# Kernel optimization log

Measured on AMD Instinct MI355X. Metric: run time of the kernel, lower is better.

The kernel has to match this reference:

```python
import jax, jax.numpy as jnp
import numpy as np

BN_EPS = 1e-5      # nn.BatchNorm1d default in MLP_Block
DICE_EPS = 1e-8    # Dice's BatchNorm eps


def _bn(x, gamma, beta, eps):
    # training-mode BatchNorm1d over the batch axis (biased variance, like torch)
    m = jnp.mean(x, axis=0)
    v = jnp.var(x, axis=0)
    return gamma * (x - m) * jax.lax.rsqrt(v + eps) + beta


def _dice(x, gamma, beta, alpha):
    gate = jax.nn.sigmoid(_bn(x, gamma, beta, DICE_EPS))
    return gate * x + (1.0 - gate) * alpha * x


def setup_inputs() -> dict:
    key = jax.random.key(0)
    ks = jax.random.split(key, 12)
    B, S, E = 4096, 200, 64
    D_in, H1, H2 = 4 * E, 64, 32
    inp = {
        "query": jax.random.normal(ks[0], (B, 1, E), jnp.float32),
        "facts": jax.random.normal(ks[1], (B, S, E), jnp.float32),
        "mask": jax.random.randint(ks[2], (B, S, 1), 0, 2).astype(jnp.int32),
        # layer 1: Linear(256->64) + BN + Dice
        "W1": jax.random.normal(ks[3], (D_in, H1), jnp.float32) / np.sqrt(D_in),
        "b1": jnp.zeros((H1,), jnp.float32),
        "g1": jnp.ones((H1,), jnp.float32),
        "be1": jnp.zeros((H1,), jnp.float32),
        "dg1": jnp.ones((H1,), jnp.float32),
        "db1": jnp.zeros((H1,), jnp.float32),
        "a1": 0.1 * jax.random.normal(ks[4], (H1,), jnp.float32),
        # layer 2: Linear(64->32) + BN + Dice
        "W2": jax.random.normal(ks[5], (H1, H2), jnp.float32) / np.sqrt(H1),
        "b2": jnp.zeros((H2,), jnp.float32),
        "g2": jnp.ones((H2,), jnp.float32),
        "be2": jnp.zeros((H2,), jnp.float32),
        "dg2": jnp.ones((H2,), jnp.float32),
        "db2": jnp.zeros((H2,), jnp.float32),
        "a2": 0.1 * jax.random.normal(ks[6], (H2,), jnp.float32),
        # final fc: Linear(32->1)
        "Wf": jax.random.normal(ks[7], (H2, 1), jnp.float32) / np.sqrt(H2),
        "bf": jnp.zeros((1,), jnp.float32),
    }
    return inp


def reference(query, facts, mask,
              W1, b1, g1, be1, dg1, db1, a1,
              W2, b2, g2, be2, dg2, db2, a2,
              Wf, bf):
    B, S, E = facts.shape
    q = jnp.broadcast_to(query, (B, S, E))
    # [B*S, 4E]
    ai = jnp.concatenate([q, facts, q - facts, q * facts], axis=-1).reshape(-1, 4 * E)
    h = ai @ W1 + b1
    h = _bn(h, g1, be1, BN_EPS)
    h = _dice(h, dg1, db1, a1)
    h = h @ W2 + b2
    h = _bn(h, g2, be2, BN_EPS)
    h = _dice(h, dg2, db2, a2)
    scores = (h @ Wf + bf).reshape(B, S, 1)
    scores = jnp.where(mask > 0, scores, jnp.float32(-1e9))
    weights = jax.nn.softmax(scores, axis=1)          # [B,S,1]
    return jnp.sum(weights * facts, axis=1)           # [B,E]
```

## Files before the change

### kernel.cpp

```cpp
#include <hip/hip_runtime.h>
#include <hip/hip_bf16.h>

#define NB 4096
#define NS 200
#define NE 64
#define NROWS (NB*NS)

typedef __attribute__((ext_vector_type(8))) short bf16x8;
typedef __attribute__((ext_vector_type(4))) float f32x4;

__device__ __forceinline__ float bf2f(unsigned v) {
    return __uint_as_float(v << 16);
}
__device__ __forceinline__ unsigned f2bf(float x) {
    unsigned u = __float_as_uint(x);
    u = u + 0x7fffu + ((u >> 16) & 1u);
    return u >> 16;
}

__global__ __launch_bounds__(256) void k_prep(const float* __restrict__ W2,
                                              float* __restrict__ stats,
                                              unsigned short* __restrict__ W2h,
                                              unsigned short* __restrict__ W2l) {
    const int t = threadIdx.x, bb = blockIdx.x;
    if (bb < 144) { stats[bb*256 + t] = 0.f; return; }
    #pragma unroll
    for (int r = 0; r < 8; ++r) {
        int idx = r*256 + t;
        int k = idx >> 5, j = idx & 31;
        float v = W2[idx];
        unsigned hb = f2bf(v);
        W2h[j*64 + k] = (unsigned short)hb;
        W2l[j*64 + k] = (unsigned short)(__float_as_uint(v - bf2f(hb)) >> 16);
    }
}

__global__ __launch_bounds__(256) void k_mq(const float* __restrict__ query,
        const float* __restrict__ W1, const float* __restrict__ b1,
        unsigned* __restrict__ Mt, float* __restrict__ qW) {
    __shared__ float qs[8][64];
    const int t = threadIdx.x;
    const int b0 = blockIdx.x * 8;
    qs[t >> 6][t & 63]       = query[(size_t)b0*64 + t];
    qs[4 + (t >> 6)][t & 63] = query[(size_t)b0*64 + 256 + t];
    __syncthreads();
    const int j = t >> 2, e0 = (t & 3) * 16;
    const int P = ((j>>5)&1)*32 + ((j>>2)&1)*16 + ((j>>3)&3)*4 + (j&3);
    float dW[16], sW[16], w3[16];
    #pragma unroll
    for (int ee = 0; ee < 16; ++ee) {
        const int e = e0 + ee;
        float w0  = W1[(size_t)e*64 + j];
        float w1v = W1[(size_t)(64+e)*64 + j];
        float w2v = W1[(size_t)(128+e)*64 + j];
        w3[ee]    = W1[(size_t)(192+e)*64 + j];
        dW[ee] = w1v - w2v;
        sW[ee] = w0 + w2v;
    }
    const float bj = b1[j];
    #pragma unroll
    for (int bb = 0; bb < 8; ++bb) {
        const int b = b0 + bb;
        float qp = 0.f;
        unsigned wbuf[8];
        #pragma unroll
        for (int ee = 0; ee < 16; ee += 2) {
            float q0 = qs[bb][e0+ee], q1 = qs[bb][e0+ee+1];
            float m0 = fmaf(q0, w3[ee],   dW[ee]);
            float m1 = fmaf(q1, w3[ee+1], dW[ee+1]);
            qp = fmaf(q0, sW[ee],   qp);
            qp = fmaf(q1, sW[ee+1], qp);
            wbuf[ee >> 1] = f2bf(m0) | (f2bf(m1) << 16);
        }
        uint4* dst = (uint4*)(Mt + (size_t)b*2048 + P*32 + (t & 3)*8);
        dst[0] = make_uint4(wbuf[0], wbuf[1], wbuf[2], wbuf[3]);
        dst[1] = make_uint4(wbuf[4], wbuf[5], wbuf[6], wbuf[7]);
        qp += __shfl_xor(qp, 1, 64);
        qp += __shfl_xor(qp, 2, 64);
        if ((t & 3) == 0) qW[(size_t)b*64 + P] = bj + qp;
    }
}

__device__ __forceinline__ void cvt_hilo(const float4& x, const float4& y,
                                         bf16x8& hi, bf16x8& lo) {
    const float f[8] = {x.x, x.y, x.z, x.w, y.x, y.y, y.z, y.w};
    #pragma unroll
    for (int i = 0; i < 8; ++i) {
        unsigned us = f2bf(f[i]);
        hi[i] = (short)us;
        lo[i] = (short)(__float_as_uint(f[i] - bf2f(us)) >> 16);
    }
}

__device__ __forceinline__ void p1_tile(
    const float4& x0, const float4& x1, const float4& x2, const float4& x3,
    const bf16x8 (&Af)[4][2], const float4 (&qw4)[4],
    int sv, bool chk, float (&sacc)[16], float (&qacc)[16],
    unsigned* __restrict__ hb, int h)
{
    bf16x8 Bh0, Bl0, Bh1, Bl1;
    cvt_hilo(x0, x1, Bh0, Bl0);
    cvt_hilo(x2, x3, Bh1, Bl1);
    f32x4 acc[4];
    #pragma unroll
    for (int cg = 0; cg < 4; ++cg) {
        acc[cg] = (f32x4){0.f,0.f,0.f,0.f};
        acc[cg] = __builtin_amdgcn_mfma_f32_16x16x32_bf16(Af[cg][0], Bh0, acc[cg], 0,0,0);
        acc[cg] = __builtin_amdgcn_mfma_f32_16x16x32_bf16(Af[cg][1], Bh1, acc[cg], 0,0,0);
        acc[cg] = __builtin_amdgcn_mfma_f32_16x16x32_bf16(Af[cg][0], Bl0, acc[cg], 0,0,0);
        acc[cg] = __builtin_amdgcn_mfma_f32_16x16x32_bf16(Af[cg][1], Bl1, acc[cg], 0,0,0);
    }
    if (!chk || sv < 200) {
        float v[4][4];
        #pragma unroll
        for (int cg = 0; cg < 4; ++cg) {
            v[cg][0] = acc[cg][0] + qw4[cg].x;
            v[cg][1] = acc[cg][1] + qw4[cg].y;
            v[cg][2] = acc[cg][2] + qw4[cg].z;
            v[cg][3] = acc[cg][3] + qw4[cg].w;
            #pragma unroll
            for (int r = 0; r < 4; ++r) {
                sacc[cg*4+r] += v[cg][r];
                qacc[cg*4+r] = fmaf(v[cg][r], v[cg][r], qacc[cg*4+r]);
            }
        }
        uint4 c0, c1;
        c0.x = f2bf(v[0][0]) | (f2bf(v[0][1]) << 16);
        c0.y = f2bf(v[0][2]) | (f2bf(v[0][3]) << 16);
        c0.z = f2bf(v[1][0]) | (f2bf(v[1][1]) << 16);
        c0.w = f2bf(v[1][2]) | (f2bf(v[1][3]) << 16);
        c1.x = f2bf(v[2][0]) | (f2bf(v[2][1]) << 16);
        c1.y = f2bf(v[2][2]) | (f2bf(v[2][3]) << 16);
        c1.z = f2bf(v[3][0]) | (f2bf(v[3][1]) << 16);
        c1.w = f2bf(v[3][2]) | (f2bf(v[3][3]) << 16);
        *(uint4*)&hb[(size_t)sv*32 + 4*h]      = c0;
        *(uint4*)&hb[(size_t)sv*32 + 16 + 4*h] = c1;
    }
}

__global__ __launch_bounds__(256) void k_p1g(const float* __restrict__ facts,
        const unsigned* __restrict__ Mt, const float* __restrict__ qW,
        float* __restrict__ gsumS, float* __restrict__ gsqS,
        unsigned* __restrict__ h1w) {
    __shared__ float sred[4][128];
    const int b = blockIdx.x, t = threadIdx.x;
    const int l = t & 63, w = t >> 6;
    const int lo4 = l & 15, h = l >> 4;

    const unsigned* mb = Mt + (size_t)b*2048;
    bf16x8 Af[4][2];
    #pragma unroll
    for (int cg = 0; cg < 4; ++cg)
        #pragma unroll
        for (int ks = 0; ks < 2; ++ks)
            Af[cg][ks] = *(const bf16x8*)&mb[(cg*16 + lo4)*32 + ks*16 + 4*h];
    float4 qw4[4];
    #pragma unroll
    for (int cg = 0; cg < 4; ++cg)
        qw4[cg] = *(const float4*)&qW[(size_t)b*64 + cg*16 + 4*h];

    const float* fb = facts + (size_t)b*(NS*NE) + 8*h;
    unsigned* hb = h1w + (size_t)b*200*32;

    float sacc[16], qacc[16];
    #pragma unroll
    for (int i = 0; i < 16; ++i) { sacc[i] = 0.f; qacc[i] = 0.f; }

#define P1L(RT, X0, X1, X2, X3, CHK) do { \
    const int sv_ = (RT)*16 + lo4; \
    if (!(CHK) || sv_ < 200) { \
        const float* p_ = fb + (size_t)sv_*64; \
        X0 = *(const float4*)(p_);      X1 = *(const float4*)(p_+4); \
        X2 = *(const float4*)(p_+32);   X3 = *(const float4*)(p_+36); \
    } else { X0 = X1 = X2 = X3 = make_float4(0.f,0.f,0.f,0.f); } \
} while(0)
#define P1P(RT, X0, X1, X2, X3, CHK) \
    p1_tile(X0, X1, X2, X3, Af, qw4, (RT)*16 + lo4, CHK, sacc, qacc, hb, h)

    float4 A0,A1,A2,A3, B0,B1,B2,B3, C0,C1,C2_,C3;
    const bool h3 = (w == 0);
    P1L(w,     A0,A1,A2,A3, false);
    P1L(w + 4, B0,B1,B2,B3, false);
    P1L(w + 8, C0,C1,C2_,C3, false);
    P1P(w,     A0,A1,A2,A3, false);
    if (h3) P1L(12, A0,A1,A2,A3, true);
    P1P(w + 4, B0,B1,B2,B3, false);
    P1P(w + 8, C0,C1,C2_,C3, false);
    if (h3) P1P(12, A0,A1,A2,A3, true);
#undef P1L
#undef P1P

    #pragma unroll
    for (int cg = 0; cg < 4; ++cg) {
        #pragma unroll
        for (int r = 0; r < 4; ++r) {
            const int i = cg*4 + r;
            float s = sacc[i], q = qacc[i];
            s += __shfl_xor(s, 1, 64); s += __shfl_xor(s, 2, 64);
            s += __shfl_xor(s, 4, 64); s += __shfl_xor(s, 8, 64);
            q += __shfl_xor(q, 1, 64); q += __shfl_xor(q, 2, 64);
            q += __shfl_xor(q, 4, 64); q += __shfl_xor(q, 8, 64);
            if (lo4 == 0) {
                const int ch = 32*(cg>>1) + 4*(cg&1) + 8*h + r;
                sred[w][ch] = s; sred[w][64 + ch] = q;
            }
        }
    }
    __syncthreads();
    if (t < 128) {
        const int slot = b & 255;
        float v = sred[0][t] + sred[1][t] + sred[2][t] + sred[3][t];
        if (t < 64) atomicAdd(gsumS + slot*64 + t, v);
        else        atomicAdd(gsqS  + slot*64 + (t - 64), v);
    }
}

__global__ __launch_bounds__(64) void k_fin(const float* __restrict__ gsumS,
        const float* __restrict__ gsqS, int S,
        const float* __restrict__ gam, const float* __restrict__ bet,
        const float* __restrict__ dg, const float* __restrict__ db,
        float* __restrict__ C, int n) {
    int j = threadIdx.x;
    if (j >= n) return;
    float sum = 0.f, sq = 0.f;
    #pragma unroll 8
    for (int s = 0; s < S; ++s) {
        sum += gsumS[s*n + j];
        sq  += gsqS[s*n + j];
    }
    const float Ninv = 1.0f / (float)NROWS;
    float m = sum * Ninv;
    float v = fmaxf(sq*Ninv - m*m, 0.f);
    float rstd = rsqrtf(v + 1e-5f);
    float A = gam[j] * rstd;
    float Bc = bet[j] - A*m;
    float vard = A*A*v;
    float rstdd = rsqrtf(vard + 1e-8f);
    float G = dg[j] * rstdd * A;
    float H = db[j] - G*m;
    C[j] = A; C[n+j] = Bc; C[2*n+j] = G; C[3*n+j] = H;
}

__device__ __forceinline__ void dice8(const bf16x8& hv, int k0, const float* Cs,
                                      bf16x8& Bh, bf16x8& Bl) {
    #pragma unroll
    for (int i = 0; i < 8; ++i) {
        const int k = k0 + i;
        float h = bf2f((unsigned short)hv[i]);
        float x  = fmaf(Cs[k],     h, Cs[64+k]);
        float tg = fmaf(Cs[128+k], h, Cs[192+k]);
        float gate = __builtin_amdgcn_rcpf(1.f + __expf(-tg));
        float fac = fmaf(gate, Cs[256+k], Cs[320+k]);
        float hd = x * fac;
        unsigned us = f2bf(hd);
        Bh[i] = (short)us;
        Bl[i] = (short)(__float_as_uint(hd - bf2f(us)) >> 16);
    }
}

__global__ __launch_bounds__(256) void k_pass2(const unsigned short* __restrict__ h1u,
        const float* __restrict__ C1, const float* __restrict__ a1,
        const unsigned short* __restrict__ W2h, const unsigned short* __restrict__ W2l,
        const float* __restrict__ b2,
        unsigned* __restrict__ h2w,
        float* __restrict__ gsum2S, float* __restrict__ gsq2S) {
    __shared__ float Cs[384];
    __shared__ float sred[4][64];
    const int t = threadIdx.x;
    const int l = t & 63, w = t >> 6;
    const int lo4 = l & 15, hi4 = l >> 4;
    Cs[t] = C1[t];
    if (t < 64) { Cs[256 + t] = 1.f - a1[t]; Cs[320 + t] = a1[t]; }
    __syncthreads();

    bf16x8 Ah[2][2], Al[2][2];
    #pragma unroll
    for (int cg = 0; cg < 2; ++cg) {
        const int col = cg*16 + lo4;
        #pragma unroll
        for (int ks = 0; ks < 2; ++ks) {
            const int k0 = ks*32 + 8*hi4;
            Ah[cg][ks] = *(const bf16x8*)&W2h[col*64 + k0];
            Al[cg][ks] = *(const bf16x8*)&W2l[col*64 + k0];
        }
    }
    float4 b24[2];
    #pragma unroll
    for (int cg = 0; cg < 2; ++cg)
        b24[cg] = *(const float4*)&b2[cg*16 + 4*hi4];

    float s2[8], q2[8];
    #pragma unroll
    for (int i = 0; i < 8; ++i) { s2[i] = 0.f; q2[i] = 0.f; }
    const int rbase0 = blockIdx.x*256 + w*64;

#define P2_LOAD(TT, H0, H1) do { \
    const int s_ = rbase0 + (TT)*16 + lo4; \
    H0 = *(const bf16x8*)&h1u[(size_t)s_*64 + 8*hi4]; \
    H1 = *(const bf16x8*)&h1u[(size_t)s_*64 + 32 + 8*hi4]; \
} while(0)

#define P2_PROC(TT, H0, H1) do { \
    bf16x8 Bh0, Bl0, Bh1, Bl1; \
    dice8(H0, 8*hi4,      Cs, Bh0, Bl0); \
    dice8(H1, 32 + 8*hi4, Cs, Bh1, Bl1); \
    f32x4 a_[2]; \
    _Pragma("unroll") \
    for (int cg = 0; cg < 2; ++cg) { \
        a_[cg] = (f32x4){0.f,0.f,0.f,0.f}; \
        a_[cg] = __builtin_amdgcn_mfma_f32_16x16x32_bf16(Ah[cg][0], Bh0, a_[cg], 0,0,0); \
        a_[cg] = __builtin_amdgcn_mfma_f32_16x16x32_bf16(Ah[cg][1], Bh1, a_[cg], 0,0,0); \
        a_[cg] = __builtin_amdgcn_mfma_f32_16x16x32_bf16(Al[cg][0], Bh0, a_[cg], 0,0,0); \
        a_[cg] = __builtin_amdgcn_mfma_f32_16x16x32_bf16(Al[cg][1], Bh1, a_[cg], 0,0,0); \
        a_[cg] = __builtin_amdgcn_mfma_f32_16x16x32_bf16(Ah[cg][0], Bl0, a_[cg], 0,0,0); \
        a_[cg] = __builtin_amdgcn_mfma_f32_16x16x32_bf16(Ah[cg][1], Bl1, a_[cg], 0,0,0); \
    } \
    const int s_ = rbase0 + (TT)*16 + lo4; \
    _Pragma("unroll") \
    for (int cg = 0; cg < 2; ++cg) { \
        float v0 = a_[cg][0] + b24[cg].x; \
        float v1 = a_[cg][1] + b24[cg].y; \
        float v2 = a_[cg][2] + b24[cg].z; \
        float v3 = a_[cg][3] + b24[cg].w; \
        s2[cg*4+0] += v0; q2[cg*4+0] = fmaf(v0, v0, q2[cg*4+0]); \
        s2[cg*4+1] += v1; q2[cg*4+1] = fmaf(v1, v1, q2[cg*4+1]); \
        s2[cg*4+2] += v2; q2[cg*4+2] = fmaf(v2, v2, q2[cg*4+2]); \
        s2[cg*4+3] += v3; q2[cg*4+3] = fmaf(v3, v3, q2[cg*4+3]); \
        uint2 pv; \
        pv.x = f2bf(v0) | (f2bf(v1) << 16); \
        pv.y = f2bf(v2) | (f2bf(v3) << 16); \
        *(uint2*)&h2w[(size_t)s_*16 + 8*cg + 2*hi4] = pv; \
    } \
} while(0)

    bf16x8 X0, X1, Y0, Y1;
    P2_LOAD(0, X0, X1);
    P2_LOAD(1, Y0, Y1);
    P2_PROC(0, X0, X1);
    P2_LOAD(2, X0, X1);
    P2_PROC(1, Y0, Y1);
    P2_LOAD(3, Y0, Y1);
    P2_PROC(2, X0, X1);
    P2_PROC(3, Y0, Y1);
#undef P2_LOAD
#undef P2_PROC

    #pragma unroll
    for (int i = 0; i < 8; ++i) {
        float s = s2[i], q = q2[i];
        s += __shfl_xor(s, 1, 64); s += __shfl_xor(s, 2, 64);
        s += __shfl_xor(s, 4, 64); s += __shfl_xor(s, 8, 64);
        q += __shfl_xor(q, 1, 64); q += __shfl_xor(q, 2, 64);
        q += __shfl_xor(q, 4, 64); q += __shfl_xor(q, 8, 64);
        if (lo4 == 0) {
            const int ch = (i >> 2)*16 + 4*hi4 + (i & 3);
            sred[w][ch] = s; sred[w][32 + ch] = q;
        }
    }
    __syncthreads();
    if (t < 64) {
        const int slot = blockIdx.x & 63;
        float v = sred[0][t] + sred[1][t] + sred[2][t] + sred[3][t];
        if (t < 32) atomicAdd(gsum2S + slot*32 + t, v);
        else        atomicAdd(gsq2S  + slot*32 + (t - 32), v);
    }
}

__device__ __forceinline__ float wsum(float v) {
    #pragma unroll
    for (int m = 32; m; m >>= 1) v += __shfl_xor(v, m, 64);
    return v;
}
__device__ __forceinline__ float wmax(float v) {
    #pragma unroll
    for (int m = 32; m; m >>= 1) v = fmaxf(v, __shfl_xor(v, m, 64));
    return v;
}
__global__ __launch_bounds__(256) void k_pass3(const unsigned* __restrict__ h2p,
        const float* __restrict__ C2, const float* __restrict__ a2,
        const float* __restrict__ Wf, const float* __restrict__ bfp,
        const int* __restrict__ mask, const float* __restrict__ facts,
        float* __restrict__ out) {
    __shared__ float rmax[4], rsum[4], wgt[256], par[4][64];
    const int b = blockIdx.x, t = threadIdx.x;
    float score = -1e30f;
    if (t < NS) {
        size_t g = (size_t)b*NS + t;
        const uint4* hv = (const uint4*)(h2p + g*16);
        uint4 U0 = hv[0], U1 = hv[1], U2 = hv[2], U3 = hv[3];
        unsigned uw[16] = {U0.x,U0.y,U0.z,U0.w, U1.x,U1.y,U1.z,U1.w,
                           U2.x,U2.y,U2.z,U2.w, U3.x,U3.y,U3.z,U3.w};
        float acc = bfp[0];
        #pragma unroll
        for (int jp = 0; jp < 16; ++jp) {
            unsigned u = uw[jp];
            #pragma unroll
            for (int h = 0; h < 2; ++h) {
                int k = 2*jp + h;
                float hval = bf2f(h ? (u >> 16) : (u & 0xffffu));
                float x  = fmaf(C2[k],    hval, C2[32+k]);
                float tg = fmaf(C2[64+k], hval, C2[96+k]);
                float gate = __builtin_amdgcn_rcpf(1.f + __expf(-tg));
                float al = a2[k];
                acc = fmaf(x * fmaf(gate, 1.f - al, al), Wf[k], acc);
            }
        }
        score = (mask[g] > 0) ? acc : -1e9f;
    }
    float m = wmax(score);
    if ((t & 63) == 0) rmax[t >> 6] = m;
    __syncthreads();
    m = fmaxf(fmaxf(rmax[0],rmax[1]), fmaxf(rmax[2],rmax[3]));
    float ee = __expf(score - m);
    float zs = wsum(ee);
    if ((t & 63) == 0) rsum[t >> 6] = zs;
    __syncthreads();
    float Z = rsum[0]+rsum[1]+rsum[2]+rsum[3];
    wgt[t] = ee * __builtin_amdgcn_rcpf(Z);
    __syncthreads();
    const int e = t & 63, p = t >> 6;
    const float* fbp = facts + (size_t)b*(NS*NE) + e;
    float a0 = 0.f, a1 = 0.f;
    #pragma unroll
    for (int i = 0; i < 200; i += 8) {
        a0 = fmaf(wgt[p + i],     fbp[(size_t)(p + i)*64],     a0);
        a1 = fmaf(wgt[p + i + 4], fbp[(size_t)(p + i + 4)*64], a1);
    }
    par[p][e] = a0 + a1;
    __syncthreads();
    if (t < 64) out[(size_t)b*64 + t] = par[0][t]+par[1][t]+par[2][t]+par[3][t];
}

extern "C" void kernel_launch(void* const* d_in, const int* in_sizes, int n_in,
                              void* d_out, int out_size, void* d_ws, size_t ws_size,
                              hipStream_t stream) {
    const float* query = (const float*)d_in[0];
    const float* facts = (const float*)d_in[1];
    const int*   mask  = (const int*)d_in[2];
    const float* W1  = (const float*)d_in[3];
    const float* b1  = (const float*)d_in[4];
    const float* g1  = (const float*)d_in[5];
    const float* be1 = (const float*)d_in[6];
    const float* dg1 = (const float*)d_in[7];
    const float* db1 = (const float*)d_in[8];
    const float* a1  = (const float*)d_in[9];
    const float* W2  = (const float*)d_in[10];
    const float* b2  = (const float*)d_in[11];
    const float* g2  = (const float*)d_in[12];
    const float* be2 = (const float*)d_in[13];
    const float* dg2 = (const float*)d_in[14];
    const float* db2 = (const float*)d_in[15];
    const float* a2  = (const float*)d_in[16];
    const float* Wf  = (const float*)d_in[17];
    const float* bff = (const float*)d_in[18];
    float* out = (float*)d_out;

    float* ws = (float*)d_ws;
    float* gsum1s = ws + 0;
    float* gsq1s  = ws + 16384;
    float* gsum2s = ws + 32768;
    float* gsq2s  = ws + 34816;
    float* C1     = ws + 36864;
    float* C2     = ws + 37120;
    unsigned short* W2h = (unsigned short*)(ws + 37376);
    unsigned short* W2l = (unsigned short*)(ws + 38400);
    unsigned* h1p = (unsigned*)(ws + 40960);
    unsigned* h2p = h1p + (size_t)NROWS*32;
    unsigned* Mt = h2p;
    float* qWb   = (float*)(h2p + (size_t)NB*2048);
    (void)ws_size; (void)in_sizes; (void)n_in; (void)out_size;

    k_prep<<<145, 256, 0, stream>>>(W2, ws, W2h, W2l);
    k_mq<<<NB/8, 256, 0, stream>>>(query, W1, b1, Mt, qWb);
    k_p1g<<<NB, 256, 0, stream>>>(facts, Mt, qWb, gsum1s, gsq1s, h1p);
    k_fin<<<1, 64, 0, stream>>>(gsum1s, gsq1s, 256, g1, be1, dg1, db1, C1, 64);
    k_pass2<<<NROWS/256, 256, 0, stream>>>((const unsigned short*)h1p, C1, a1,
                                           W2h, W2l, b2,
                                           h2p, gsum2s, gsq2s);
    k_fin<<<1, 32, 0, stream>>>(gsum2s, gsq2s, 64, g2, be2, dg2, db2, C2, 32);
    k_pass3<<<NB, 256, 0, stream>>>(h2p, C2, a2, Wf, bff, mask, facts, out);
}
```

Baseline: 217.0 us.

## Recompute layer-1 activations in pass 2 instead of storing h1

The first pass now only accumulates BatchNorm statistics for layer 1 and no longer writes the bf16 h1 intermediate. The second pass re-reads facts per batch, recomputes the layer-1 matmul with MFMA, applies BN+Dice, and then does layer 2. This trades the write and re-read of h1 (about 105 MB each way) for an extra read of facts (about 210 MB) plus duplicated MFMA and conversion work. The workspace layout shrinks accordingly.

```diff
diff --git a/kernel.cpp b/kernel.cpp
--- a/kernel.cpp
+++ b/kernel.cpp
@@ -92,11 +92,10 @@
     }
 }
 
-__device__ __forceinline__ void p1_tile(
+__device__ __forceinline__ void p1s_tile(
     const float4& x0, const float4& x1, const float4& x2, const float4& x3,
-    const bf16x8 (&Af)[4][2], const float4 (&qw4)[4],
-    int sv, bool chk, float (&sacc)[16], float (&qacc)[16],
-    unsigned* __restrict__ hb, int h)
+    const bf16x8 (&Af)[4][2], const f32x4 (&qw4)[4],
+    int sv, bool chk, float (&sacc)[16], float (&qacc)[16])
 {
     bf16x8 Bh0, Bl0, Bh1, Bl1;
     cvt_hilo(x0, x1, Bh0, Bl0);
@@ -111,37 +110,21 @@
         acc[cg] = __builtin_amdgcn_mfma_f32_16x16x32_bf16(Af[cg][1], Bl1, acc[cg], 0,0,0);
     }
     if (!chk || sv < 200) {
-        float v[4][4];
         #pragma unroll
         for (int cg = 0; cg < 4; ++cg) {
-            v[cg][0] = acc[cg][0] + qw4[cg].x;
-            v[cg][1] = acc[cg][1] + qw4[cg].y;
-            v[cg][2] = acc[cg][2] + qw4[cg].z;
-            v[cg][3] = acc[cg][3] + qw4[cg].w;
             #pragma unroll
             for (int r = 0; r < 4; ++r) {
-                sacc[cg*4+r] += v[cg][r];
-                qacc[cg*4+r] = fmaf(v[cg][r], v[cg][r], qacc[cg*4+r]);
+                float v = acc[cg][r] + qw4[cg][r];
+                sacc[cg*4+r] += v;
+                qacc[cg*4+r] = fmaf(v, v, qacc[cg*4+r]);
             }
         }
-        uint4 c0, c1;
-        c0.x = f2bf(v[0][0]) | (f2bf(v[0][1]) << 16);
-        c0.y = f2bf(v[0][2]) | (f2bf(v[0][3]) << 16);
-        c0.z = f2bf(v[1][0]) | (f2bf(v[1][1]) << 16);
-        c0.w = f2bf(v[1][2]) | (f2bf(v[1][3]) << 16);
-        c1.x = f2bf(v[2][0]) | (f2bf(v[2][1]) << 16);
-        c1.y = f2bf(v[2][2]) | (f2bf(v[2][3]) << 16);
-        c1.z = f2bf(v[3][0]) | (f2bf(v[3][1]) << 16);
-        c1.w = f2bf(v[3][2]) | (f2bf(v[3][3]) << 16);
-        *(uint4*)&hb[(size_t)sv*32 + 4*h]      = c0;
-        *(uint4*)&hb[(size_t)sv*32 + 16 + 4*h] = c1;
-    }
-}
-
-__global__ __launch_bounds__(256) void k_p1g(const float* __restrict__ facts,
+    }
+}
+
+__global__ __launch_bounds__(256) void k_p1s(const float* __restrict__ facts,
         const unsigned* __restrict__ Mt, const float* __restrict__ qW,
-        float* __restrict__ gsumS, float* __restrict__ gsqS,
-        unsigned* __restrict__ h1w) {
+        float* __restrict__ gsumS, float* __restrict__ gsqS) {
     __shared__ float sred[4][128];
     const int b = blockIdx.x, t = threadIdx.x;
     const int l = t & 63, w = t >> 6;
@@ -154,13 +137,12 @@
         #pragma unroll
         for (int ks = 0; ks < 2; ++ks)
             Af[cg][ks] = *(const bf16x8*)&mb[(cg*16 + lo4)*32 + ks*16 + 4*h];
-    float4 qw4[4];
+    f32x4 qw4[4];
     #pragma unroll
     for (int cg = 0; cg < 4; ++cg)
-        qw4[cg] = *(const float4*)&qW[(size_t)b*64 + cg*16 + 4*h];
+        qw4[cg] = *(const f32x4*)&qW[(size_t)b*64 + cg*16 + 4*h];
 
     const float* fb = facts + (size_t)b*(NS*NE) + 8*h;
-    unsigned* hb = h1w + (size_t)b*200*32;
 
     float sacc[16], qacc[16];
     #pragma unroll
@@ -175,7 +157,7 @@
     } else { X0 = X1 = X2 = X3 = make_float4(0.f,0.f,0.f,0.f); } \
 } while(0)
 #define P1P(RT, X0, X1, X2, X3, CHK) \
-    p1_tile(X0, X1, X2, X3, Af, qw4, (RT)*16 + lo4, CHK, sacc, qacc, hb, h)
+    p1s_tile(X0, X1, X2, X3, Af, qw4, (RT)*16 + lo4, CHK, sacc, qacc)
 
     float4 A0,A1,A2,A3, B0,B1,B2,B3, C0,C1,C2_,C3;
     const bool h3 = (w == 0);
@@ -241,24 +223,8 @@
     C[j] = A; C[n+j] = Bc; C[2*n+j] = G; C[3*n+j] = H;
 }
 
-__device__ __forceinline__ void dice8(const bf16x8& hv, int k0, const float* Cs,
-                                      bf16x8& Bh, bf16x8& Bl) {
-    #pragma unroll
-    for (int i = 0; i < 8; ++i) {
-        const int k = k0 + i;
-        float h = bf2f((unsigned short)hv[i]);
-        float x  = fmaf(Cs[k],     h, Cs[64+k]);
-        float tg = fmaf(Cs[128+k], h, Cs[192+k]);
-        float gate = __builtin_amdgcn_rcpf(1.f + __expf(-tg));
-        float fac = fmaf(gate, Cs[256+k], Cs[320+k]);
-        float hd = x * fac;
-        unsigned us = f2bf(hd);
-        Bh[i] = (short)us;
-        Bl[i] = (short)(__float_as_uint(hd - bf2f(us)) >> 16);
-    }
-}
-
-__global__ __launch_bounds__(256) void k_pass2(const unsigned short* __restrict__ h1u,
+__global__ __launch_bounds__(256) void k_p2f(const float* __restrict__ facts,
+        const unsigned* __restrict__ Mt, const float* __restrict__ qW,
         const float* __restrict__ C1, const float* __restrict__ a1,
         const unsigned short* __restrict__ W2h, const unsigned short* __restrict__ W2l,
         const float* __restrict__ b2,
@@ -266,84 +232,137 @@
         float* __restrict__ gsum2S, float* __restrict__ gsq2S) {
     __shared__ float Cs[384];
     __shared__ float sred[4][64];
-    const int t = threadIdx.x;
+    const int b = blockIdx.x, t = threadIdx.x;
     const int l = t & 63, w = t >> 6;
-    const int lo4 = l & 15, hi4 = l >> 4;
+    const int lo4 = l & 15, h = l >> 4;
     Cs[t] = C1[t];
     if (t < 64) { Cs[256 + t] = 1.f - a1[t]; Cs[320 + t] = a1[t]; }
     __syncthreads();
 
-    bf16x8 Ah[2][2], Al[2][2];
+    const unsigned* mb = Mt + (size_t)b*2048;
+    bf16x8 Af[4][2];
+    #pragma unroll
+    for (int cg = 0; cg < 4; ++cg)
+        #pragma unroll
+        for (int ks = 0; ks < 2; ++ks)
+            Af[cg][ks] = *(const bf16x8*)&mb[(cg*16 + lo4)*32 + ks*16 + 4*h];
+    f32x4 qw4[4];
+    #pragma unroll
+    for (int cg = 0; cg < 4; ++cg)
+        qw4[cg] = *(const f32x4*)&qW[(size_t)b*64 + cg*16 + 4*h];
+
+    bf16x8 Wh[2][2], Wl[2][2];
     #pragma unroll
     for (int cg = 0; cg < 2; ++cg) {
         const int col = cg*16 + lo4;
         #pragma unroll
         for (int ks = 0; ks < 2; ++ks) {
-            const int k0 = ks*32 + 8*hi4;
-            Ah[cg][ks] = *(const bf16x8*)&W2h[col*64 + k0];
-            Al[cg][ks] = *(const bf16x8*)&W2l[col*64 + k0];
-        }
-    }
-    float4 b24[2];
+            const int k0 = ks*32 + 8*h;
+            Wh[cg][ks] = *(const bf16x8*)&W2h[col*64 + k0];
+            Wl[cg][ks] = *(const bf16x8*)&W2l[col*64 + k0];
+        }
+    }
+    f32x4 b24[2];
     #pragma unroll
     for (int cg = 0; cg < 2; ++cg)
-        b24[cg] = *(const float4*)&b2[cg*16 + 4*hi4];
+        b24[cg] = *(const f32x4*)&b2[cg*16 + 4*h];
+
+    const float* fb = facts + (size_t)b*(NS*NE) + 8*h;
+    unsigned* h2b = h2w + (size_t)b*200*16;
 
     float s2[8], q2[8];
     #pragma unroll
     for (int i = 0; i < 8; ++i) { s2[i] = 0.f; q2[i] = 0.f; }
-    const int rbase0 = blockIdx.x*256 + w*64;
-
-#define P2_LOAD(TT, H0, H1) do { \
-    const int s_ = rbase0 + (TT)*16 + lo4; \
-    H0 = *(const bf16x8*)&h1u[(size_t)s_*64 + 8*hi4]; \
-    H1 = *(const bf16x8*)&h1u[(size_t)s_*64 + 32 + 8*hi4]; \
+
+#define P2L(RT, X0, X1, X2, X3, CHK) do { \
+    const int sv_ = (RT)*16 + lo4; \
+    if (!(CHK) || sv_ < 200) { \
+        const float* p_ = fb + (size_t)sv_*64; \
+        X0 = *(const float4*)(p_);      X1 = *(const float4*)(p_+4); \
+        X2 = *(const float4*)(p_+32);   X3 = *(const float4*)(p_+36); \
+    } else { X0 = X1 = X2 = X3 = make_float4(0.f,0.f,0.f,0.f); } \
 } while(0)
 
-#define P2_PROC(TT, H0, H1) do { \
-    bf16x8 Bh0, Bl0, Bh1, Bl1; \
-    dice8(H0, 8*hi4,      Cs, Bh0, Bl0); \
-    dice8(H1, 32 + 8*hi4, Cs, Bh1, Bl1); \
+#define P2P(RT, X0, X1, X2, X3, CHK) do { \
+    bf16x8 Fh0, Fl0, Fh1, Fl1; \
+    cvt_hilo(X0, X1, Fh0, Fl0); \
+    cvt_hilo(X2, X3, Fh1, Fl1); \
+    f32x4 acc[4]; \
+    _Pragma("unroll") \
+    for (int cg = 0; cg < 4; ++cg) { \
+        acc[cg] = (f32x4){0.f,0.f,0.f,0.f}; \
+        acc[cg] = __builtin_amdgcn_mfma_f32_16x16x32_bf16(Af[cg][0], Fh0, acc[cg], 0,0,0); \
+        acc[cg] = __builtin_amdgcn_mfma_f32_16x16x32_bf16(Af[cg][1], Fh1, acc[cg], 0,0,0); \
+        acc[cg] = __builtin_amdgcn_mfma_f32_16x16x32_bf16(Af[cg][0], Fl0, acc[cg], 0,0,0); \
+        acc[cg] = __builtin_amdgcn_mfma_f32_16x16x32_bf16(Af[cg][1], Fl1, acc[cg], 0,0,0); \
+    } \
+    bf16x8 H0h, H0l, H1h, H1l; \
+    _Pragma("unroll") \
+    for (int cg = 0; cg < 4; ++cg) { \
+        const int cb = 32*(cg>>1) + 4*(cg&1) + 8*h; \
+        f32x4 Ac = *(const f32x4*)&Cs[cb]; \
+        f32x4 Bc = *(const f32x4*)&Cs[64+cb]; \
+        f32x4 Gc = *(const f32x4*)&Cs[128+cb]; \
+        f32x4 Hc = *(const f32x4*)&Cs[192+cb]; \
+        f32x4 Oc = *(const f32x4*)&Cs[256+cb]; \
+        f32x4 Lc = *(const f32x4*)&Cs[320+cb]; \
+        _Pragma("unroll") \
+        for (int r = 0; r < 4; ++r) { \
+            float hv = acc[cg][r] + qw4[cg][r]; \
+            float x  = fmaf(Ac[r], hv, Bc[r]); \
+            float tg = fmaf(Gc[r], hv, Hc[r]); \
+            float gate = __builtin_amdgcn_rcpf(1.f + __expf(-tg)); \
+            float hd = x * fmaf(gate, Oc[r], Lc[r]); \
+            unsigned us = f2bf(hd); \
+            unsigned lo = __float_as_uint(hd - bf2f(us)) >> 16; \
+            const int idx = 4*(cg&1) + r; \
+            if (cg < 2) { H0h[idx] = (short)us; H0l[idx] = (short)lo; } \
+            else        { H1h[idx] = (short)us; H1l[idx] = (short)lo; } \
+        } \
+    } \
     f32x4 a_[2]; \
     _Pragma("unroll") \
     for (int cg = 0; cg < 2; ++cg) { \
         a_[cg] = (f32x4){0.f,0.f,0.f,0.f}; \
-        a_[cg] = __builtin_amdgcn_mfma_f32_16x16x32_bf16(Ah[cg][0], Bh0, a_[cg], 0,0,0); \
-        a_[cg] = __builtin_amdgcn_mfma_f32_16x16x32_bf16(Ah[cg][1], Bh1, a_[cg], 0,0,0); \
-        a_[cg] = __builtin_amdgcn_mfma_f32_16x16x32_bf16(Al[cg][0], Bh0, a_[cg], 0,0,0); \
-        a_[cg] = __builtin_amdgcn_mfma_f32_16x16x32_bf16(Al[cg][1], Bh1, a_[cg], 0,0,0); \
-        a_[cg] = __builtin_amdgcn_mfma_f32_16x16x32_bf16(Ah[cg][0], Bl0, a_[cg], 0,0,0); \
-        a_[cg] = __builtin_amdgcn_mfma_f32_16x16x32_bf16(Ah[cg][1], Bl1, a_[cg], 0,0,0); \
+        a_[cg] = __builtin_amdgcn_mfma_f32_16x16x32_bf16(Wh[cg][0], H0h, a_[cg], 0,0,0); \
+        a_[cg] = __builtin_amdgcn_mfma_f32_16x16x32_bf16(Wh[cg][1], H1h, a_[cg], 0,0,0); \
+        a_[cg] = __builtin_amdgcn_mfma_f32_16x16x32_bf16(Wl[cg][0], H0h, a_[cg], 0,0,0); \
+        a_[cg] = __builtin_amdgcn_mfma_f32_16x16x32_bf16(Wl[cg][1], H1h, a_[cg], 0,0,0); \
+        a_[cg] = __builtin_amdgcn_mfma_f32_16x16x32_bf16(Wh[cg][0], H0l, a_[cg], 0,0,0); \
+        a_[cg] = __builtin_amdgcn_mfma_f32_16x16x32_bf16(Wh[cg][1], H1l, a_[cg], 0,0,0); \
     } \
-    const int s_ = rbase0 + (TT)*16 + lo4; \
-    _Pragma("unroll") \
-    for (int cg = 0; cg < 2; ++cg) { \
-        float v0 = a_[cg][0] + b24[cg].x; \
-        float v1 = a_[cg][1] + b24[cg].y; \
-        float v2 = a_[cg][2] + b24[cg].z; \
-        float v3 = a_[cg][3] + b24[cg].w; \
-        s2[cg*4+0] += v0; q2[cg*4+0] = fmaf(v0, v0, q2[cg*4+0]); \
-        s2[cg*4+1] += v1; q2[cg*4+1] = fmaf(v1, v1, q2[cg*4+1]); \
-        s2[cg*4+2] += v2; q2[cg*4+2] = fmaf(v2, v2, q2[cg*4+2]); \
-        s2[cg*4+3] += v3; q2[cg*4+3] = fmaf(v3, v3, q2[cg*4+3]); \
-        uint2 pv; \
-        pv.x = f2bf(v0) | (f2bf(v1) << 16); \
-        pv.y = f2bf(v2) | (f2bf(v3) << 16); \
-        *(uint2*)&h2w[(size_t)s_*16 + 8*cg + 2*hi4] = pv; \
+    const int sv_ = (RT)*16 + lo4; \
+    if (!(CHK) || sv_ < 200) { \
+        _Pragma("unroll") \
+        for (int cg = 0; cg < 2; ++cg) { \
+            float v0 = a_[cg][0] + b24[cg][0]; \
+            float v1 = a_[cg][1] + b24[cg][1]; \
+            float v2 = a_[cg][2] + b24[cg][2]; \
+            float v3 = a_[cg][3] + b24[cg][3]; \
+            s2[cg*4+0] += v0; q2[cg*4+0] = fmaf(v0, v0, q2[cg*4+0]); \
+            s2[cg*4+1] += v1; q2[cg*4+1] = fmaf(v1, v1, q2[cg*4+1]); \
+            s2[cg*4+2] += v2; q2[cg*4+2] = fmaf(v2, v2, q2[cg*4+2]); \
+            s2[cg*4+3] += v3; q2[cg*4+3] = fmaf(v3, v3, q2[cg*4+3]); \
+            uint2 pv; \
+            pv.x = f2bf(v0) | (f2bf(v1) << 16); \
+            pv.y = f2bf(v2) | (f2bf(v3) << 16); \
+            *(uint2*)&h2b[(size_t)sv_*16 + 8*cg + 2*h] = pv; \
+        } \
     } \
 } while(0)
 
-    bf16x8 X0, X1, Y0, Y1;
-    P2_LOAD(0, X0, X1);
-    P2_LOAD(1, Y0, Y1);
-    P2_PROC(0, X0, X1);
-    P2_LOAD(2, X0, X1);
-    P2_PROC(1, Y0, Y1);
-    P2_LOAD(3, Y0, Y1);
-    P2_PROC(2, X0, X1);
-    P2_PROC(3, Y0, Y1);
-#undef P2_LOAD
-#undef P2_PROC
+    float4 A0,A1,A2,A3, B0,B1,B2,B3;
+    const bool h3 = (w == 0);
+    P2L(w,     A0,A1,A2,A3, false);
+    P2L(w + 4, B0,B1,B2,B3, false);
+    P2P(w,     A0,A1,A2,A3, false);
+    P2L(w + 8, A0,A1,A2,A3, false);
+    P2P(w + 4, B0,B1,B2,B3, false);
+    if (h3) P2L(12, B0,B1,B2,B3, true);
+    P2P(w + 8, A0,A1,A2,A3, false);
+    if (h3) P2P(12, B0,B1,B2,B3, true);
+#undef P2L
+#undef P2P
 
     #pragma unroll
     for (int i = 0; i < 8; ++i) {
@@ -353,13 +372,13 @@
         q += __shfl_xor(q, 1, 64); q += __shfl_xor(q, 2, 64);
         q += __shfl_xor(q, 4, 64); q += __shfl_xor(q, 8, 64);
         if (lo4 == 0) {
-            const int ch = (i >> 2)*16 + 4*hi4 + (i & 3);
+            const int ch = (i >> 2)*16 + 4*h + (i & 3);
             sred[w][ch] = s; sred[w][32 + ch] = q;
         }
     }
     __syncthreads();
     if (t < 64) {
-        const int slot = blockIdx.x & 63;
+        const int slot = b & 63;
         float v = sred[0][t] + sred[1][t] + sred[2][t] + sred[3][t];
         if (t < 32) atomicAdd(gsum2S + slot*32 + t, v);
         else        atomicAdd(gsq2S  + slot*32 + (t - 32), v);
@@ -464,19 +483,17 @@
     float* C2     = ws + 37120;
     unsigned short* W2h = (unsigned short*)(ws + 37376);
     unsigned short* W2l = (unsigned short*)(ws + 38400);
-    unsigned* h1p = (unsigned*)(ws + 40960);
-    unsigned* h2p = h1p + (size_t)NROWS*32;
-    unsigned* Mt = h2p;
-    float* qWb   = (float*)(h2p + (size_t)NB*2048);
+    unsigned* Mt  = (unsigned*)(ws + 40960);
+    float* qWb    = (float*)(Mt + (size_t)NB*2048);
+    unsigned* h2p = (unsigned*)(qWb + (size_t)NB*64);
     (void)ws_size; (void)in_sizes; (void)n_in; (void)out_size;
 
     k_prep<<<145, 256, 0, stream>>>(W2, ws, W2h, W2l);
     k_mq<<<NB/8, 256, 0, stream>>>(query, W1, b1, Mt, qWb);
-    k_p1g<<<NB, 256, 0, stream>>>(facts, Mt, qWb, gsum1s, gsq1s, h1p);
+    k_p1s<<<NB, 256, 0, stream>>>(facts, Mt, qWb, gsum1s, gsq1s);
     k_fin<<<1, 64, 0, stream>>>(gsum1s, gsq1s, 256, g1, be1, dg1, db1, C1, 64);
-    k_pass2<<<NROWS/256, 256, 0, stream>>>((const unsigned short*)h1p, C1, a1,
-                                           W2h, W2l, b2,
-                                           h2p, gsum2s, gsq2s);
+    k_p2f<<<NB, 256, 0, stream>>>(facts, Mt, qWb, C1, a1, W2h, W2l, b2,
+                                  h2p, gsum2s, gsq2s);
     k_fin<<<1, 32, 0, stream>>>(gsum2s, gsq2s, 64, g2, be2, dg2, db2, C2, 32);
     k_pass3<<<NB, 256, 0, stream>>>(h2p, C2, a2, Wf, bff, mask, facts, out);
 }
```

Result: slower. 289.7 us (+33.5%).
